# Kernel optimization log

Measured on AMD Instinct MI355X. Metric: run time of the kernel, lower is better.

Reference implementation:

```python
import jax, jax.numpy as jnp
import numpy as np

N_POINTS = 200
LEVEL_DIM = 4
NUM_LEVELS = 3
RESOLUTIONS = (8, 16, 32)  # base_resolution=8, per-level scale 2
BATCH = 32768


def _sph_to_cart(theta, phi):
    st = jnp.sin(theta)
    return jnp.stack([st * jnp.cos(phi), st * jnp.sin(phi), jnp.cos(theta)], axis=-1)


def _sample_points(x):
    # x: [B,4] -> points on segment between two unit-sphere points: [B, N_POINTS, 3]
    p1 = _sph_to_cart(x[:, 0], x[:, 1])
    p2 = _sph_to_cart(x[:, 2], x[:, 3])
    t = jnp.linspace(0.0, 1.0, N_POINTS, dtype=x.dtype).reshape(1, N_POINTS, 1)
    return p1[:, None, :] + (p2 - p1)[:, None, :] * t


def _grid_interp(points, table, R):
    # points: [B,S,3] in [-1,1]; table: [(R+1)^3, D] dense grid. Trilinear interp.
    u = jnp.clip((points + 1.0) * 0.5, 0.0, 1.0) * R
    p0 = jnp.clip(jnp.floor(u).astype(jnp.int32), 0, R - 1)
    f = u - p0.astype(u.dtype)
    Rp1 = R + 1
    out = jnp.zeros(points.shape[:-1] + (table.shape[-1],), dtype=table.dtype)
    for c in range(8):  # fixed 8 trilinear corners
        off = np.array([(c >> 2) & 1, (c >> 1) & 1, c & 1], dtype=np.int32)
        idx = p0 + off
        lin = (idx[..., 0] * Rp1 + idx[..., 1]) * Rp1 + idx[..., 2]
        w = jnp.prod(jnp.where(off == 1, f, 1.0 - f), axis=-1)
        out = out + w[..., None] * table[lin]
    return out


def setup_inputs() -> dict:
    key = jax.random.key(0)
    ks = jax.random.split(key, 8)
    pi = 3.14159265
    x = jax.random.uniform(ks[0], (BATCH, 4), dtype=jnp.float32) * pi
    grid0 = jax.random.normal(ks[1], ((RESOLUTIONS[0] + 1) ** 3, LEVEL_DIM), jnp.float32) * 0.1
    grid1 = jax.random.normal(ks[2], ((RESOLUTIONS[1] + 1) ** 3, LEVEL_DIM), jnp.float32) * 0.1
    grid2 = jax.random.normal(ks[3], ((RESOLUTIONS[2] + 1) ** 3, LEVEL_DIM), jnp.float32) * 0.1
    w_label = jax.random.normal(ks[4], (NUM_LEVELS, 1), jnp.float32) * 0.5
    b_label = jnp.zeros((1,), jnp.float32)
    w_rgb = jax.random.normal(ks[5], (NUM_LEVELS * (LEVEL_DIM - 1), 3), jnp.float32) * 0.3
    b_rgb = jnp.zeros((3,), jnp.float32)
    return {"x": x, "grid0": grid0, "grid1": grid1, "grid2": grid2,
            "w_label": w_label, "b_label": b_label, "w_rgb": w_rgb, "b_rgb": b_rgb}


def reference(x, grid0, grid1, grid2, w_label, b_label, w_rgb, b_rgb):
    # torch wraps ray sampling in no_grad -> stop_gradient
    points = jax.lax.stop_gradient(_sample_points(x))  # [B,S,3]
    enc = jnp.concatenate(
        [_grid_interp(points, g, R) for g, R in zip((grid0, grid1, grid2), RESOLUTIONS)],
        axis=-1)  # [B,S,12]
    labels_in = enc[:, :, ::LEVEL_DIM]                      # [B,S,3]
    all_prob = jax.nn.sigmoid(labels_in @ w_label + b_label)  # [B,S,1]
    output_hits = jnp.max(all_prob, axis=1)                 # [B,1]
    mask = np.ones(NUM_LEVELS * LEVEL_DIM, dtype=bool)
    mask[::LEVEL_DIM] = False
    rgb_feats = enc[:, :, mask]                             # [B,S,9]
    hit = (all_prob > 0.5).astype(enc.dtype)
    idx_first = jnp.argmax(hit, axis=1)                     # [B,1] first sample with prob>0.5 (0 if none)
    idx3 = jnp.broadcast_to(idx_first[:, :, None], (rgb_feats.shape[0], 1, rgb_feats.shape[2]))
    gathered = jnp.take_along_axis(rgb_feats, idx3, axis=1)[:, 0, :]  # [B,9]
    output_rgb = jax.nn.sigmoid(gathered @ w_rgb + b_rgb)   # [B,3]
    return (output_hits, output_rgb)
```

## Files before the change

kernel.cpp:

```cpp
#include <hip/hip_runtime.h>
#include <math.h>

#define NPTS 200
#define L33   33
#define L33SQ 1089
#define NLAT  35937

template<int R>
__device__ __forceinline__ float tri_label(const float* __restrict__ g,
                                           float ux, float uy, float uz) {
    constexpr int Rp1 = R + 1;
    constexpr int SX  = Rp1 * Rp1;
    int ix = min((int)ux, R - 1);
    int iy = min((int)uy, R - 1);
    int iz = min((int)uz, R - 1);
    float fx = ux - (float)ix, fy = uy - (float)iy, fz = uz - (float)iz;
    int b = (ix * Rp1 + iy) * Rp1 + iz;
    float v000 = g[4*b],            v001 = g[4*(b+1)];
    float v010 = g[4*(b+Rp1)],      v011 = g[4*(b+Rp1+1)];
    float v100 = g[4*(b+SX)],       v101 = g[4*(b+SX+1)];
    float v110 = g[4*(b+SX+Rp1)],   v111 = g[4*(b+SX+Rp1+1)];
    float c00 = fmaf(fz, v001 - v000, v000);
    float c01 = fmaf(fz, v011 - v010, v010);
    float c10 = fmaf(fz, v101 - v100, v100);
    float c11 = fmaf(fz, v111 - v110, v110);
    float c0  = fmaf(fy, c01 - c00, c00);
    float c1  = fmaf(fy, c11 - c10, c10);
    return fmaf(fx, c1 - c0, c0);
}

__global__ __launch_bounds__(128)
void prep1_kernel(const float* __restrict__ g0, const float* __restrict__ g1,
                  const float* __restrict__ g2, const float* __restrict__ wl,
                  const float* __restrict__ bl, float* __restrict__ T) {
    int i = blockIdx.x * blockDim.x + threadIdx.x;
    if (i >= NLAT) return;
    int jz = i % L33;
    int r  = i / L33;
    int jy = r % L33;
    int jx = r / L33;
    float fx = (float)jx, fy = (float)jy, fz = (float)jz;
    float L0 = tri_label<8 >(g0, fx * 0.25f, fy * 0.25f, fz * 0.25f);
    float L1 = tri_label<16>(g1, fx * 0.5f,  fy * 0.5f,  fz * 0.5f);
    float L2 = g2[4 * i];
    T[i] = bl[0] + wl[0] * L0 + wl[1] * L1 + wl[2] * L2;
}

template<int R>
__device__ __forceinline__ void rgb_corner(const float* __restrict__ g,
                                           float cx, float cy, float cz,
                                           int dx, int dy, int dz,
                                           float* f3) {
    constexpr int Rp1 = R + 1;
    float ux = cx * (float)R, uy = cy * (float)R, uz = cz * (float)R;
    int ix = min((int)ux, R - 1);
    int iy = min((int)uy, R - 1);
    int iz = min((int)uz, R - 1);
    float fx = ux - (float)ix, fy = uy - (float)iy, fz = uz - (float)iz;
    int idx = ((ix + dx) * Rp1 + (iy + dy)) * Rp1 + (iz + dz);
    float w = (dx ? fx : 1.0f - fx) * (dy ? fy : 1.0f - fy) * (dz ? fz : 1.0f - fz);
    float4 v = *reinterpret_cast<const float4*>(g + 4 * idx);
    f3[0] = w * v.y;
    f3[1] = w * v.z;
    f3[2] = w * v.w;
}

__global__ __launch_bounds__(1024, 4)
void rays_kernel(const float* __restrict__ x,
                 const float* __restrict__ T,
                 const float* __restrict__ g0,
                 const float* __restrict__ g1,
                 const float* __restrict__ g2,
                 const float* __restrict__ wr,
                 const float* __restrict__ br,
                 float* __restrict__ out_hits,
                 float* __restrict__ out_rgb)
{
    extern __shared__ float Tl[];
    const int tid = (int)threadIdx.x;

    for (int i = tid; i < NLAT; i += 1024) Tl[i] = T[i];
    __syncthreads();

    const int ray = (int)blockIdx.x * 128 + (tid >> 3);
    const int sub = tid & 7;

    const float th1 = x[ray * 4 + 0];
    const float ph1 = x[ray * 4 + 1];
    const float th2 = x[ray * 4 + 2];
    const float ph2 = x[ray * 4 + 3];
    float s1 = __sinf(th1), c1 = __cosf(th1);
    float s2 = __sinf(th2), c2 = __cosf(th2);
    float p1x = s1 * __cosf(ph1), p1y = s1 * __sinf(ph1), p1z = c1;
    float p2x = s2 * __cosf(ph2), p2y = s2 * __sinf(ph2), p2z = c2;
    const float dxr = p2x - p1x, dyr = p2y - p1y, dzr = p2z - p1z;

    const float inv = 1.0f / (float)(NPTS - 1);
    const float sc  = 16.0f * inv;

    const float bx = fmaf(p1x, 16.0f, 16.0f);
    const float by = fmaf(p1y, 16.0f, 16.0f);
    const float bz = fmaf(p1z, 16.0f, 16.0f);
    const float dux = dxr * sc, duy = dyr * sc, duz = dzr * sc;

    const float subf = (float)sub;
    float maxlogit = -INFINITY;
    unsigned hmask = 0u;

#pragma unroll
    for (int i = 0; i < 25; ++i) {
        float tf = subf + (float)(8 * i);
        float ux = fmaf(tf, dux, bx);
        float uy = fmaf(tf, duy, by);
        float uz = fmaf(tf, duz, bz);
        int ix = min((int)ux, 31);
        int iy = min((int)uy, 31);
        int iz = min((int)uz, 31);
        float fx = ux - (float)ix;
        float fy = uy - (float)iy;
        float fz = uz - (float)iz;
        int b = (ix * L33 + iy) * L33 + iz;
        float v000 = Tl[b],               v001 = Tl[b + 1];
        float v010 = Tl[b + L33],         v011 = Tl[b + L33 + 1];
        float v100 = Tl[b + L33SQ],       v101 = Tl[b + L33SQ + 1];
        float v110 = Tl[b + L33SQ + L33], v111 = Tl[b + L33SQ + L33 + 1];
        float a00 = fmaf(fz, v001 - v000, v000);
        float a01 = fmaf(fz, v011 - v010, v010);
        float a10 = fmaf(fz, v101 - v100, v100);
        float a11 = fmaf(fz, v111 - v110, v110);
        float b0  = fmaf(fy, a01 - a00, a00);
        float b1  = fmaf(fy, a11 - a10, a10);
        float logit = fmaf(fx, b1 - b0, b0);
        maxlogit = fmaxf(maxlogit, logit);
        hmask |= (logit > 0.0f) ? (1u << i) : 0u;
    }

    int fc = hmask ? (8 * __builtin_ctz(hmask) + sub) : NPTS;

#pragma unroll
    for (int m = 4; m >= 1; m >>= 1) {
        maxlogit = fmaxf(maxlogit, __shfl_xor(maxlogit, m, 64));
        fc = min(fc, __shfl_xor(fc, m, 64));
    }

    const int tsel = (fc >= NPTS) ? 0 : fc;
    {
        float tt = (float)tsel * inv;
        float px = fmaf(dxr, tt, p1x);
        float py = fmaf(dyr, tt, p1y);
        float pz = fmaf(dzr, tt, p1z);
        float cx = fminf(fmaxf(fmaf(px, 0.5f, 0.5f), 0.0f), 1.0f);
        float cy = fminf(fmaxf(fmaf(py, 0.5f, 0.5f), 0.0f), 1.0f);
        float cz = fminf(fmaxf(fmaf(pz, 0.5f, 0.5f), 0.0f), 1.0f);
        const int dx = (sub >> 2) & 1, dy = (sub >> 1) & 1, dz = sub & 1;
        float feat[9];
        rgb_corner<8 >(g0, cx, cy, cz, dx, dy, dz, &feat[0]);
        rgb_corner<16>(g1, cx, cy, cz, dx, dy, dz, &feat[3]);
        rgb_corner<32>(g2, cx, cy, cz, dx, dy, dz, &feat[6]);
        float acc[3];
#pragma unroll
        for (int c = 0; c < 3; ++c) {
            float a = 0.0f;
#pragma unroll
            for (int f = 0; f < 9; ++f) a = fmaf(feat[f], wr[f * 3 + c], a);
            acc[c] = a;
        }
#pragma unroll
        for (int m = 4; m >= 1; m >>= 1) {
#pragma unroll
            for (int c = 0; c < 3; ++c)
                acc[c] += __shfl_xor(acc[c], m, 64);
        }
        if (sub == 0) {
            out_hits[ray] = 1.0f / (1.0f + __expf(-maxlogit));
#pragma unroll
            for (int c = 0; c < 3; ++c)
                out_rgb[ray * 3 + c] = 1.0f / (1.0f + __expf(-(acc[c] + br[c])));
        }
    }
}

extern "C" void kernel_launch(void* const* d_in, const int* in_sizes, int n_in,
                              void* d_out, int out_size, void* d_ws, size_t ws_size,
                              hipStream_t stream) {
    const float* x  = (const float*)d_in[0];
    const float* g0 = (const float*)d_in[1];
    const float* g1 = (const float*)d_in[2];
    const float* g2 = (const float*)d_in[3];
    const float* wl = (const float*)d_in[4];
    const float* bl = (const float*)d_in[5];
    const float* wr = (const float*)d_in[6];
    const float* br = (const float*)d_in[7];

    const int n = in_sizes[0] / 4;
    float* out_hits = (float*)d_out;
    float* out_rgb  = (float*)d_out + n;

    float* T = (float*)d_ws;

    prep1_kernel<<<(NLAT + 127) / 128, 128, 0, stream>>>(g0, g1, g2, wl, bl, T);

    const int grid = n / 128;
    rays_kernel<<<grid, 1024, NLAT * sizeof(float), stream>>>(
        x, T, g0, g1, g2, wr, br, out_hits, out_rgb);
}
```

Measured before the change: 21.89 us.

## Split label-grid lookups between LDS and a packed global float4 table

The prep kernel now also builds a packed table in which each entry stores the four (y,z) corner values as a float4, laid out x-fastest. Odd sample steps in the ray loop read two float4 values from global memory (through the cache) instead of making eight LDS reads. The intent is to spread lookup traffic across the LDS and L1/L2 paths so that LDS bandwidth is no longer the only bottleneck. Launch bounds drop to 2 blocks per CU, and the workspace grows to hold the 4x-sized table.

```diff
diff --git a/kernel.cpp b/kernel.cpp
--- a/kernel.cpp
+++ b/kernel.cpp
@@ -5,6 +5,9 @@
 #define L33   33
 #define L33SQ 1089
 #define NLAT  35937
+#define NPREP (NLAT * 4)
+
+#define WS_T_OFF_FLOATS (NLAT * 4)
 
 template<int R>
 __device__ __forceinline__ float tri_label(const float* __restrict__ g,
@@ -29,21 +32,28 @@
     return fmaf(fx, c1 - c0, c0);
 }
 
-__global__ __launch_bounds__(128)
-void prep1_kernel(const float* __restrict__ g0, const float* __restrict__ g1,
-                  const float* __restrict__ g2, const float* __restrict__ wl,
-                  const float* __restrict__ bl, float* __restrict__ T) {
-    int i = blockIdx.x * blockDim.x + threadIdx.x;
-    if (i >= NLAT) return;
-    int jz = i % L33;
-    int r  = i / L33;
-    int jy = r % L33;
-    int jx = r / L33;
-    float fx = (float)jx, fy = (float)jy, fz = (float)jz;
+__global__ __launch_bounds__(256)
+void prep_kernel(const float* __restrict__ g0, const float* __restrict__ g1,
+                 const float* __restrict__ g2, const float* __restrict__ wl,
+                 const float* __restrict__ bl, float* __restrict__ Pf,
+                 float* __restrict__ T) {
+    int id = blockIdx.x * blockDim.x + threadIdx.x;
+    if (id >= NPREP) return;
+    int c  = id & 3;
+    int jj = id >> 2;
+    int ix = jj % L33;
+    int r  = jj / L33;
+    int iz = r % L33;
+    int iy = r / L33;
+    int jy = min(iy + (c >> 1), L33 - 1);
+    int jz = min(iz + (c & 1),  L33 - 1);
+    float fx = (float)ix, fy = (float)jy, fz = (float)jz;
     float L0 = tri_label<8 >(g0, fx * 0.25f, fy * 0.25f, fz * 0.25f);
     float L1 = tri_label<16>(g1, fx * 0.5f,  fy * 0.5f,  fz * 0.5f);
-    float L2 = g2[4 * i];
-    T[i] = bl[0] + wl[0] * L0 + wl[1] * L1 + wl[2] * L2;
+    float L2 = g2[4 * ((ix * L33 + jy) * L33 + jz)];
+    float v = bl[0] + wl[0] * L0 + wl[1] * L1 + wl[2] * L2;
+    Pf[id] = v;
+    if (c == 0) T[(ix * L33 + iy) * L33 + iz] = v;
 }
 
 template<int R>
@@ -65,9 +75,10 @@
     f3[2] = w * v.w;
 }
 
-__global__ __launch_bounds__(1024, 4)
+__global__ __launch_bounds__(1024, 2)
 void rays_kernel(const float* __restrict__ x,
                  const float* __restrict__ T,
+                 const float4* __restrict__ P,
                  const float* __restrict__ g0,
                  const float* __restrict__ g1,
                  const float* __restrict__ g2,
@@ -119,18 +130,33 @@
         float fx = ux - (float)ix;
         float fy = uy - (float)iy;
         float fz = uz - (float)iz;
-        int b = (ix * L33 + iy) * L33 + iz;
-        float v000 = Tl[b],               v001 = Tl[b + 1];
-        float v010 = Tl[b + L33],         v011 = Tl[b + L33 + 1];
-        float v100 = Tl[b + L33SQ],       v101 = Tl[b + L33SQ + 1];
-        float v110 = Tl[b + L33SQ + L33], v111 = Tl[b + L33SQ + L33 + 1];
-        float a00 = fmaf(fz, v001 - v000, v000);
-        float a01 = fmaf(fz, v011 - v010, v010);
-        float a10 = fmaf(fz, v101 - v100, v100);
-        float a11 = fmaf(fz, v111 - v110, v110);
-        float b0  = fmaf(fy, a01 - a00, a00);
-        float b1  = fmaf(fy, a11 - a10, a10);
-        float logit = fmaf(fx, b1 - b0, b0);
+        float logit;
+        if ((i & 1) == 0) {
+            int b = (ix * L33 + iy) * L33 + iz;
+            float v000 = Tl[b],               v001 = Tl[b + 1];
+            float v010 = Tl[b + L33],         v011 = Tl[b + L33 + 1];
+            float v100 = Tl[b + L33SQ],       v101 = Tl[b + L33SQ + 1];
+            float v110 = Tl[b + L33SQ + L33], v111 = Tl[b + L33SQ + L33 + 1];
+            float a00 = fmaf(fz, v001 - v000, v000);
+            float a01 = fmaf(fz, v011 - v010, v010);
+            float a10 = fmaf(fz, v101 - v100, v100);
+            float a11 = fmaf(fz, v111 - v110, v110);
+            float b0  = fmaf(fy, a01 - a00, a00);
+            float b1  = fmaf(fy, a11 - a10, a10);
+            logit = fmaf(fx, b1 - b0, b0);
+        } else {
+            int jj = (iy * L33 + iz) * L33 + ix;
+            const float4* p = P + jj;
+            float4 q0 = p[0];
+            float4 q1 = p[1];
+            float mx = fmaf(fx, q1.x - q0.x, q0.x);
+            float my = fmaf(fx, q1.y - q0.y, q0.y);
+            float mz = fmaf(fx, q1.z - q0.z, q0.z);
+            float mw = fmaf(fx, q1.w - q0.w, q0.w);
+            float r0 = fmaf(fz, my - mx, mx);
+            float r1 = fmaf(fz, mw - mz, mz);
+            logit = fmaf(fy, r1 - r0, r0);
+        }
         maxlogit = fmaxf(maxlogit, logit);
         hmask |= (logit > 0.0f) ? (1u << i) : 0u;
     }
@@ -196,11 +222,12 @@
     float* out_hits = (float*)d_out;
     float* out_rgb  = (float*)d_out + n;
 
-    float* T = (float*)d_ws;
-
-    prep1_kernel<<<(NLAT + 127) / 128, 128, 0, stream>>>(g0, g1, g2, wl, bl, T);
+    float* Pf = (float*)d_ws;
+    float* T  = (float*)d_ws + WS_T_OFF_FLOATS;
+
+    prep_kernel<<<(NPREP + 255) / 256, 256, 0, stream>>>(g0, g1, g2, wl, bl, Pf, T);
 
     const int grid = n / 128;
     rays_kernel<<<grid, 1024, NLAT * sizeof(float), stream>>>(
-        x, T, g0, g1, g2, wr, br, out_hits, out_rgb);
-}
+        x, T, (const float4*)Pf, g0, g1, g2, wr, br, out_hits, out_rgb);
+}
```

Result: no change. 21.74 us (-0.7%).
